# Optimization experiments

Measured on AMD Instinct MI355X. Metric: run time of the kernel, lower is better.

The kernel has to match this reference:

```python
import jax, jax.numpy as jnp
import numpy as np

B, V, F, O = 256, 512, 256, 2


def setup_inputs() -> dict:
    key = jax.random.key(0)
    k1, k2, k3, k4, k5, k6 = jax.random.split(key, 6)
    features = jax.random.normal(k1, (B, V, F), dtype=jnp.float32)
    graphs = jax.random.randint(k2, (B, V, V), 0, 2, dtype=jnp.int32)
    # GCNConv params: lin (no bias) weight [F, O] + separate bias [O]
    conv_weight = jax.random.normal(k3, (F, O), dtype=jnp.float32) / np.sqrt(F)
    conv_bias = jax.random.normal(k4, (O,), dtype=jnp.float32) * 0.01
    # head: Linear(O*V, 1)
    lin_weight = jax.random.normal(k5, (1, O * V), dtype=jnp.float32) / np.sqrt(O * V)
    lin_bias = jax.random.normal(k6, (1,), dtype=jnp.float32) * 0.01
    return {"features": features, "graphs": graphs, "conv_weight": conv_weight,
            "conv_bias": conv_bias, "lin_weight": lin_weight, "lin_bias": lin_bias}


def reference(features, graphs, conv_weight, conv_bias, lin_weight, lin_bias):
    # dense_to_sparse -> binary edges (edge values discarded, weight 1)
    adj = (graphs != 0).astype(features.dtype)  # [B, V, V]
    # gcn_norm: add remaining self-loops (diag = 1), symmetric normalization
    eye = jnp.eye(V, dtype=features.dtype)
    adj = jnp.where(eye > 0, 1.0, adj)
    deg = adj.sum(axis=-1)  # [B, V]
    dinv = jnp.where(deg > 0, jax.lax.rsqrt(jnp.maximum(deg, 1e-30)), 0.0)
    norm_adj = dinv[:, :, None] * adj * dinv[:, None, :]  # D^-1/2 (A+I) D^-1/2
    # GCNConv: aggregate then affine (order commutes): A_hat X W + b
    h = jnp.einsum("bvw,bwf,fo->bvo", norm_adj, features, conv_weight) + conv_bias
    h = jax.nn.relu(h).reshape(B, V * O)  # flatten(start_dim=1) of [B, V, O]
    logits = h @ lin_weight.T + lin_bias  # [B, 1]
    return jax.nn.sigmoid(logits)
```

## Files before the change

### kernel.cpp

```cpp
#include <hip/hip_runtime.h>

#define Bn 256
#define Vn 512
#define Fn 256

#define WS_PACKED_OFF 0
#define WS_DINV_OFF   8388608
#define WS_Y_OFF      8912896

__global__ __launch_bounds__(256) void fused_pack_xw_kernel(
    const int* __restrict__ G,
    const float* __restrict__ X,
    const float* __restrict__ W,
    unsigned long long* __restrict__ P,
    float* __restrict__ dinv,
    float2* __restrict__ Y) {
  int gid  = blockIdx.x * 256 + threadIdx.x;
  int row  = gid >> 6;
  int lane = gid & 63;
  int v    = row & (Vn - 1);

  const int4* g4 = (const int4*)(G + (size_t)row * Vn);
  int4 A0 = g4[lane];
  int4 A1 = g4[64 + lane];

  const float4* xr = (const float4*)(X + (size_t)row * Fn);
  float4 x = xr[lane];
  const float4* wr = (const float4*)W;
  float4 w0 = wr[lane * 2];
  float4 w1 = wr[lane * 2 + 1];

  unsigned long long m0 = __ballot(A0.x != 0);
  unsigned long long m1 = __ballot(A0.y != 0);
  unsigned long long m2 = __ballot(A0.z != 0);
  unsigned long long m3 = __ballot(A0.w != 0);
  unsigned long long m4 = __ballot(A1.x != 0);
  unsigned long long m5 = __ballot(A1.y != 0);
  unsigned long long m6 = __ballot(A1.z != 0);
  unsigned long long m7 = __ballot(A1.w != 0);

  int widx = ((v >> 8) << 2) | (v & 3);
  unsigned long long db = 1ull << ((v >> 2) & 63);
  if      (widx == 0) m0 |= db;
  else if (widx == 1) m1 |= db;
  else if (widx == 2) m2 |= db;
  else if (widx == 3) m3 |= db;
  else if (widx == 4) m4 |= db;
  else if (widx == 5) m5 |= db;
  else if (widx == 6) m6 |= db;
  else                m7 |= db;

  int deg = __popcll(m0) + __popcll(m1) + __popcll(m2) + __popcll(m3) +
            __popcll(m4) + __popcll(m5) + __popcll(m6) + __popcll(m7);

  float s0 = x.x * w0.x + x.y * w0.z + x.z * w1.x + x.w * w1.z;
  float s1 = x.x * w0.y + x.y * w0.w + x.z * w1.y + x.w * w1.w;
  #pragma unroll
  for (int off = 32; off; off >>= 1) {
    s0 += __shfl_xor(s0, off);
    s1 += __shfl_xor(s1, off);
  }

  unsigned long long sel = m0;
  sel = (lane == 1) ? m1 : sel;
  sel = (lane == 2) ? m2 : sel;
  sel = (lane == 3) ? m3 : sel;
  sel = (lane == 4) ? m4 : sel;
  sel = (lane == 5) ? m5 : sel;
  sel = (lane == 6) ? m6 : sel;
  sel = (lane == 7) ? m7 : sel;
  if (lane < 8) P[(size_t)row * 8 + lane] = sel;
  if (lane == 0) {
    dinv[row] = rsqrtf((float)deg);
    Y[row] = make_float2(s0, s1);
  }
}

__global__ __launch_bounds__(512) void agg_head_kernel(
    const unsigned long long* __restrict__ P,
    const float* __restrict__ dinv,
    const float2* __restrict__ Y,
    const float* __restrict__ lw,
    const float* __restrict__ lb,
    const float* __restrict__ cb,
    float* __restrict__ out) {
  __shared__ float2 ylds[Vn];
  __shared__ float wsum[8];

  int b = blockIdx.x;
  int t = threadIdx.x;

  float d;
  {
    d = dinv[b * Vn + t];
    float2 y = Y[b * Vn + t];
    ylds[t] = make_float2(y.x * d, y.y * d);
  }
  __syncthreads();

  const ulonglong2* p2 = (const ulonglong2*)(P + ((size_t)b * Vn + t) * 8);

  float a0 = 0.f, a1 = 0.f;
  for (int jj = 0; jj < 4; ++jj) {
    ulonglong2 mm = p2[jj];
    #pragma unroll
    for (int h = 0; h < 2; ++h) {
      unsigned long long m = h ? mm.y : mm.x;
      int j = jj * 2 + h;
      const float2* base = ylds + ((j >> 2) << 8) + (j & 3);
      unsigned lo = (unsigned)m;
      unsigned hi = (unsigned)(m >> 32);
      #pragma unroll
      for (int k = 0; k < 32; ++k) {
        float s = (float)((lo >> k) & 1u);
        float2 y = base[4 * k];
        a0 = fmaf(s, y.x, a0);
        a1 = fmaf(s, y.y, a1);
      }
      #pragma unroll
      for (int k = 0; k < 32; ++k) {
        float s = (float)((hi >> k) & 1u);
        float2 y = base[4 * k + 128];
        a0 = fmaf(s, y.x, a0);
        a1 = fmaf(s, y.y, a1);
      }
    }
  }

  float cb0 = cb[0], cb1 = cb[1];
  const float2* lw2 = (const float2*)lw;
  float2 wv = lw2[t];

  float h0 = fmaxf(fmaf(d, a0, cb0), 0.f);
  float h1 = fmaxf(fmaf(d, a1, cb1), 0.f);
  float c = h0 * wv.x + h1 * wv.y;

  #pragma unroll
  for (int off = 32; off; off >>= 1) c += __shfl_xor(c, off);
  if ((t & 63) == 0) wsum[t >> 6] = c;
  __syncthreads();
  if (t == 0) {
    float logit = wsum[0] + wsum[1] + wsum[2] + wsum[3] +
                  wsum[4] + wsum[5] + wsum[6] + wsum[7] + lb[0];
    out[b] = 1.0f / (1.0f + expf(-logit));
  }
}

extern "C" void kernel_launch(void* const* d_in, const int* in_sizes, int n_in,
                              void* d_out, int out_size, void* d_ws, size_t ws_size,
                              hipStream_t stream) {
  const float* features = (const float*)d_in[0];
  const int*   graphs   = (const int*)d_in[1];
  const float* conv_w   = (const float*)d_in[2];
  const float* conv_b   = (const float*)d_in[3];
  const float* lin_w    = (const float*)d_in[4];
  const float* lin_b    = (const float*)d_in[5];
  float* out = (float*)d_out;

  char* ws = (char*)d_ws;
  unsigned long long* P = (unsigned long long*)(ws + WS_PACKED_OFF);
  float*  dinv = (float*)(ws + WS_DINV_OFF);
  float2* Y    = (float2*)(ws + WS_Y_OFF);

  fused_pack_xw_kernel<<<dim3(32768), dim3(256), 0, stream>>>(
      graphs, features, conv_w, P, dinv, Y);
  agg_head_kernel<<<dim3(Bn), dim3(512), 0, stream>>>(
      P, dinv, Y, lin_w, lin_b, conv_b, out);
}
```

Measured before the change: 442.1 us.

## Fuse adjacency packing, XW projection and aggregation head into one kernel

```diff
diff --git a/kernel.cpp b/kernel.cpp
--- a/kernel.cpp
+++ b/kernel.cpp
@@ -4,144 +4,132 @@
 #define Vn 512
 #define Fn 256
 
-#define WS_PACKED_OFF 0
-#define WS_DINV_OFF   8388608
-#define WS_Y_OFF      8912896
-
-__global__ __launch_bounds__(256) void fused_pack_xw_kernel(
+__global__ __launch_bounds__(1024) void fused_gcn_kernel(
     const int* __restrict__ G,
     const float* __restrict__ X,
     const float* __restrict__ W,
-    unsigned long long* __restrict__ P,
-    float* __restrict__ dinv,
-    float2* __restrict__ Y) {
-  int gid  = blockIdx.x * 256 + threadIdx.x;
-  int row  = gid >> 6;
-  int lane = gid & 63;
-  int v    = row & (Vn - 1);
+    const float* __restrict__ lw,
+    const float* __restrict__ lb,
+    const float* __restrict__ cb,
+    float* __restrict__ out) {
+  __shared__ unsigned long long Plds[Vn][8];
+  __shared__ float2 ylds[Vn];
+  __shared__ float  dlds[Vn];
+  __shared__ float  wsum[16];
 
-  const int4* g4 = (const int4*)(G + (size_t)row * Vn);
-  int4 A0 = g4[lane];
-  int4 A1 = g4[64 + lane];
+  int b    = blockIdx.x;
+  int t    = threadIdx.x;
+  int wave = t >> 6;
+  int lane = t & 63;
 
-  const float4* xr = (const float4*)(X + (size_t)row * Fn);
-  float4 x = xr[lane];
   const float4* wr = (const float4*)W;
   float4 w0 = wr[lane * 2];
   float4 w1 = wr[lane * 2 + 1];
 
-  unsigned long long m0 = __ballot(A0.x != 0);
-  unsigned long long m1 = __ballot(A0.y != 0);
-  unsigned long long m2 = __ballot(A0.z != 0);
-  unsigned long long m3 = __ballot(A0.w != 0);
-  unsigned long long m4 = __ballot(A1.x != 0);
-  unsigned long long m5 = __ballot(A1.y != 0);
-  unsigned long long m6 = __ballot(A1.z != 0);
-  unsigned long long m7 = __ballot(A1.w != 0);
+  for (int it = 0; it < 32; ++it) {
+    int v = (it << 4) | wave;
+    size_t row = (size_t)b * Vn + v;
 
-  int widx = ((v >> 8) << 2) | (v & 3);
-  unsigned long long db = 1ull << ((v >> 2) & 63);
-  if      (widx == 0) m0 |= db;
-  else if (widx == 1) m1 |= db;
-  else if (widx == 2) m2 |= db;
-  else if (widx == 3) m3 |= db;
-  else if (widx == 4) m4 |= db;
-  else if (widx == 5) m5 |= db;
-  else if (widx == 6) m6 |= db;
-  else                m7 |= db;
+    const int4* g4 = (const int4*)(G + row * Vn);
+    int4 A0 = g4[lane];
+    int4 A1 = g4[64 + lane];
+    const float4* xr = (const float4*)(X + row * Fn);
+    float4 x = xr[lane];
 
-  int deg = __popcll(m0) + __popcll(m1) + __popcll(m2) + __popcll(m3) +
-            __popcll(m4) + __popcll(m5) + __popcll(m6) + __popcll(m7);
+    unsigned long long m0 = __ballot(A0.x != 0);
+    unsigned long long m1 = __ballot(A0.y != 0);
+    unsigned long long m2 = __ballot(A0.z != 0);
+    unsigned long long m3 = __ballot(A0.w != 0);
+    unsigned long long m4 = __ballot(A1.x != 0);
+    unsigned long long m5 = __ballot(A1.y != 0);
+    unsigned long long m6 = __ballot(A1.z != 0);
+    unsigned long long m7 = __ballot(A1.w != 0);
 
-  float s0 = x.x * w0.x + x.y * w0.z + x.z * w1.x + x.w * w1.z;
-  float s1 = x.x * w0.y + x.y * w0.w + x.z * w1.y + x.w * w1.w;
-  #pragma unroll
-  for (int off = 32; off; off >>= 1) {
-    s0 += __shfl_xor(s0, off);
-    s1 += __shfl_xor(s1, off);
-  }
+    int widx = ((v >> 8) << 2) | (v & 3);
+    unsigned long long db = 1ull << ((v >> 2) & 63);
+    if      (widx == 0) m0 |= db;
+    else if (widx == 1) m1 |= db;
+    else if (widx == 2) m2 |= db;
+    else if (widx == 3) m3 |= db;
+    else if (widx == 4) m4 |= db;
+    else if (widx == 5) m5 |= db;
+    else if (widx == 6) m6 |= db;
+    else                m7 |= db;
 
-  unsigned long long sel = m0;
-  sel = (lane == 1) ? m1 : sel;
-  sel = (lane == 2) ? m2 : sel;
-  sel = (lane == 3) ? m3 : sel;
-  sel = (lane == 4) ? m4 : sel;
-  sel = (lane == 5) ? m5 : sel;
-  sel = (lane == 6) ? m6 : sel;
-  sel = (lane == 7) ? m7 : sel;
-  if (lane < 8) P[(size_t)row * 8 + lane] = sel;
-  if (lane == 0) {
-    dinv[row] = rsqrtf((float)deg);
-    Y[row] = make_float2(s0, s1);
-  }
-}
+    int deg = __popcll(m0) + __popcll(m1) + __popcll(m2) + __popcll(m3) +
+              __popcll(m4) + __popcll(m5) + __popcll(m6) + __popcll(m7);
 
-__global__ __launch_bounds__(512) void agg_head_kernel(
-    const unsigned long long* __restrict__ P,
-    const float* __restrict__ dinv,
-    const float2* __restrict__ Y,
-    const float* __restrict__ lw,
-    const float* __restrict__ lb,
-    const float* __restrict__ cb,
-    float* __restrict__ out) {
-  __shared__ float2 ylds[Vn];
-  __shared__ float wsum[8];
+    float s0 = x.x * w0.x + x.y * w0.z + x.z * w1.x + x.w * w1.z;
+    float s1 = x.x * w0.y + x.y * w0.w + x.z * w1.y + x.w * w1.w;
+    #pragma unroll
+    for (int off = 32; off; off >>= 1) {
+      s0 += __shfl_xor(s0, off);
+      s1 += __shfl_xor(s1, off);
+    }
 
-  int b = blockIdx.x;
-  int t = threadIdx.x;
-
-  float d;
-  {
-    d = dinv[b * Vn + t];
-    float2 y = Y[b * Vn + t];
-    ylds[t] = make_float2(y.x * d, y.y * d);
+    unsigned long long sel = m0;
+    sel = (lane == 1) ? m1 : sel;
+    sel = (lane == 2) ? m2 : sel;
+    sel = (lane == 3) ? m3 : sel;
+    sel = (lane == 4) ? m4 : sel;
+    sel = (lane == 5) ? m5 : sel;
+    sel = (lane == 6) ? m6 : sel;
+    sel = (lane == 7) ? m7 : sel;
+    if (lane < 8) Plds[v][lane] = sel;
+    if (lane == 0) {
+      float d = rsqrtf((float)deg);
+      dlds[v] = d;
+      ylds[v] = make_float2(s0 * d, s1 * d);
+    }
   }
   __syncthreads();
 
-  const ulonglong2* p2 = (const ulonglong2*)(P + ((size_t)b * Vn + t) * 8);
-
+  int r = t >> 1;
+  int h = t & 1;
   float a0 = 0.f, a1 = 0.f;
-  for (int jj = 0; jj < 4; ++jj) {
-    ulonglong2 mm = p2[jj];
+  const float2* ybase = ylds + (h << 8);
+  #pragma unroll
+  for (int c = 0; c < 4; ++c) {
+    unsigned long long m = Plds[r][(h << 2) | c];
+    unsigned lo = (unsigned)m;
+    unsigned hi = (unsigned)(m >> 32);
+    const float2* base = ybase + c;
     #pragma unroll
-    for (int h = 0; h < 2; ++h) {
-      unsigned long long m = h ? mm.y : mm.x;
-      int j = jj * 2 + h;
-      const float2* base = ylds + ((j >> 2) << 8) + (j & 3);
-      unsigned lo = (unsigned)m;
-      unsigned hi = (unsigned)(m >> 32);
-      #pragma unroll
-      for (int k = 0; k < 32; ++k) {
-        float s = (float)((lo >> k) & 1u);
-        float2 y = base[4 * k];
-        a0 = fmaf(s, y.x, a0);
-        a1 = fmaf(s, y.y, a1);
-      }
-      #pragma unroll
-      for (int k = 0; k < 32; ++k) {
-        float s = (float)((hi >> k) & 1u);
-        float2 y = base[4 * k + 128];
-        a0 = fmaf(s, y.x, a0);
-        a1 = fmaf(s, y.y, a1);
-      }
+    for (int k = 0; k < 32; ++k) {
+      float s = (float)((lo >> k) & 1u);
+      float2 y = base[4 * k];
+      a0 = fmaf(s, y.x, a0);
+      a1 = fmaf(s, y.y, a1);
+    }
+    #pragma unroll
+    for (int k = 0; k < 32; ++k) {
+      float s = (float)((hi >> k) & 1u);
+      float2 y = base[4 * k + 128];
+      a0 = fmaf(s, y.x, a0);
+      a1 = fmaf(s, y.y, a1);
     }
   }
+  a0 += __shfl_xor(a0, 1);
+  a1 += __shfl_xor(a1, 1);
 
-  float cb0 = cb[0], cb1 = cb[1];
-  const float2* lw2 = (const float2*)lw;
-  float2 wv = lw2[t];
-
-  float h0 = fmaxf(fmaf(d, a0, cb0), 0.f);
-  float h1 = fmaxf(fmaf(d, a1, cb1), 0.f);
-  float c = h0 * wv.x + h1 * wv.y;
-
+  float c_acc = 0.f;
+  if (h == 0) {
+    float d = dlds[r];
+    float cb0 = cb[0], cb1 = cb[1];
+    const float2* lw2 = (const float2*)lw;
+    float2 wv = lw2[r];
+    float h0 = fmaxf(fmaf(d, a0, cb0), 0.f);
+    float h1 = fmaxf(fmaf(d, a1, cb1), 0.f);
+    c_acc = h0 * wv.x + h1 * wv.y;
+  }
   #pragma unroll
-  for (int off = 32; off; off >>= 1) c += __shfl_xor(c, off);
-  if ((t & 63) == 0) wsum[t >> 6] = c;
+  for (int off = 32; off; off >>= 1) c_acc += __shfl_xor(c_acc, off);
+  if (lane == 0) wsum[wave] = c_acc;
   __syncthreads();
   if (t == 0) {
-    float logit = wsum[0] + wsum[1] + wsum[2] + wsum[3] +
-                  wsum[4] + wsum[5] + wsum[6] + wsum[7] + lb[0];
+    float logit = lb[0];
+    #pragma unroll
+    for (int i = 0; i < 16; ++i) logit += wsum[i];
     out[b] = 1.0f / (1.0f + expf(-logit));
   }
 }
@@ -156,14 +144,8 @@
   const float* lin_w    = (const float*)d_in[4];
   const float* lin_b    = (const float*)d_in[5];
   float* out = (float*)d_out;
+  (void)d_ws; (void)ws_size;
 
-  char* ws = (char*)d_ws;
-  unsigned long long* P = (unsigned long long*)(ws + WS_PACKED_OFF);
-  float*  dinv = (float*)(ws + WS_DINV_OFF);
-  float2* Y    = (float2*)(ws + WS_Y_OFF);
-
-  fused_pack_xw_kernel<<<dim3(32768), dim3(256), 0, stream>>>(
-      graphs, features, conv_w, P, dinv, Y);
-  agg_head_kernel<<<dim3(Bn), dim3(512), 0, stream>>>(
-      P, dinv, Y, lin_w, lin_b, conv_b, out);
+  fused_gcn_kernel<<<dim3(Bn), dim3(1024), 0, stream>>>(
+      graphs, features, conv_w, lin_w, lin_b, conv_b, out);
 }
```

Result: slower. 512.5 us (+15.9%).
